# Kernel tuning notes

Hardware: AMD Instinct MI355X
Metric: run time of the kernel (lower is better)

## Reference

```python
import jax, jax.numpy as jnp
import numpy as np

THRESHOLD = 1.0
SLOPE = 25.0  # snntorch surrogate.fast_sigmoid default slope
BETA = 0.9

@jax.custom_vjp
def spike_fn(x):
    # Heaviside forward, fast-sigmoid surrogate backward: g / (slope*|x| + 1)^2
    return (x > 0).astype(x.dtype)

def _spike_fwd(x):
    return spike_fn(x), x

def _spike_bwd(x, g):
    return (g / (SLOPE * jnp.abs(x) + 1.0) ** 2,)

spike_fn.defvjp(_spike_fwd, _spike_bwd)


def setup_inputs() -> dict:
    key = jax.random.key(0)
    k_x, k_w1, k_b1, k_w2, k_b2 = jax.random.split(key, 5)
    B, T, F, H, O = 128, 256, 2500, 128, 2
    x = jax.random.normal(k_x, (B, T, F), dtype=jnp.float32)
    # PyTorch Linear init: U(-1/sqrt(fan_in), 1/sqrt(fan_in))
    s1 = 1.0 / np.sqrt(F)
    s2 = 1.0 / np.sqrt(H)
    W1 = jax.random.uniform(k_w1, (H, F), jnp.float32, -s1, s1)
    b1 = jax.random.uniform(k_b1, (H,), jnp.float32, -s1, s1)
    W2 = jax.random.uniform(k_w2, (O, H), jnp.float32, -s2, s2)
    b2 = jax.random.uniform(k_b2, (O,), jnp.float32, -s2, s2)
    return {"x": x, "W1": W1, "b1": b1, "W2": W2, "b2": b2}


def reference(x, W1, b1, W2, b2):
    # Module transposes to [time, batch, feat] when shape[0] < shape[1]
    if x.ndim == 3 and x.shape[0] < x.shape[1]:
        x = jnp.swapaxes(x, 0, 1)  # [T, B, F]
    T, B = x.shape[0], x.shape[1]
    H, O = W1.shape[0], W2.shape[0]

    def lif(mem, cur):
        # snntorch Leaky, reset_mechanism='subtract'; reset spike is detached
        rst = jax.lax.stop_gradient(spike_fn(mem - THRESHOLD))
        mem = BETA * mem + cur - rst * THRESHOLD
        spk = spike_fn(mem - THRESHOLD)
        return spk, mem

    def step(carry, xt):
        mem1, mem2 = carry
        cur1 = xt @ W1.T + b1            # [B, H]
        spk1, mem1 = lif(mem1, cur1)
        cur2 = spk1 @ W2.T + b2          # [B, O]
        spk2, mem2 = lif(mem2, cur2)
        return (mem1, mem2), (spk2, mem2)

    mem1_0 = jnp.zeros((B, H), x.dtype)
    mem2_0 = jnp.zeros((B, O), x.dtype)
    _, (spk_rec, mem_rec) = jax.lax.scan(step, (mem1_0, mem2_0), x)
    return spk_rec, mem_rec  # each [T, B, O]
```

## Files before the change

kernel.cpp:

```cpp
#include <hip/hip_runtime.h>
#include <hip/hip_bf16.h>

#define T_STEPS 256
#define B_SZ    128
#define F_SZ    2500
#define F4      625
#define NSTEP   79
#define H_SZ    128
#define O_SZ    2
#define FLAG_WINDOW 8e-5
#define CHUNK   12

typedef unsigned short U16;
typedef short  s16x8 __attribute__((ext_vector_type(8)));
typedef U16    u16x8 __attribute__((ext_vector_type(8)));
typedef float  f32x4 __attribute__((ext_vector_type(4)));

__device__ __forceinline__ U16 bf16c(float f) {
    union { __hip_bfloat16 h; U16 u; } cv;
    cv.h = __float2bfloat16(f);
    return cv.u;
}
__device__ __forceinline__ float bf2f(U16 u) { return __uint_as_float((unsigned)u << 16); }

__device__ __forceinline__ void gld16(const void* g, void* l) {
    __builtin_amdgcn_global_load_lds((const __attribute__((address_space(1))) void*)g,
                                     (__attribute__((address_space(3))) void*)l, 16, 0, 0);
}

__global__ __launch_bounds__(256) void k_split(const float* __restrict__ W1,
                                               U16* __restrict__ Wimg,
                                               int* __restrict__ nh) {
    const int bid = blockIdx.x;
    const int p = bid / NSTEP, kt = bid - p * NSTEP;
    if (bid == 0 && threadIdx.x < B_SZ) nh[threadIdx.x] = 0;
    U16* img = Wimg + ((size_t)bid << 12);
    #pragma unroll
    for (int c = 0; c < 2; ++c) {
        const int v  = c * 256 + threadIdx.x;
        const int r  = v >> 3, u = v & 7;
        const int lu = u ^ (r & 7);
        const int kb = kt * 32 + (lu & 3) * 8;
        const int h  = p * 64 + r;
        u16x8 o;
        #pragma unroll
        for (int e = 0; e < 8; ++e) {
            const int k = kb + e;
            const float w = (k < F_SZ) ? W1[(size_t)h * F_SZ + k] : 0.f;
            const U16 hi = bf16c(w);
            o[e] = (lu < 4) ? hi : bf16c(w - bf2f(hi));
        }
        *(u16x8*)(img + (size_t)v * 8) = o;
    }
}

__global__ __launch_bounds__(256, 3) void k_gemm(const float* __restrict__ x,
                                                 const U16* __restrict__ Wimg,
                                                 float* __restrict__ cur1) {
    __shared__ __align__(16) U16 Alds[2][128 * 64];
    __shared__ __align__(16) U16 Blds[2][64 * 64];

    const int g   = blockIdx.x;
    const int wg  = (g & 7) * 128 + (g >> 3);
    const int t   = wg >> 2;
    const int p   = (wg >> 1) & 1;
    const int kh  = wg & 1;
    const int kt0 = kh ? 40 : 0;
    const int nst = kh ? 39 : 40;

    const int tid = threadIdx.x;

    const int ra   = tid >> 1;
    const int kq   = (tid & 1) << 4;
    const int au0  = (tid & 1) << 1;
    const int aswz = ra & 7;
    const float* xrow = x + ((size_t)ra * T_STEPS + t) * F_SZ;

    const char* wbase = (const char*)Wimg + ((size_t)p * NSTEP << 13);

    const int lane = tid & 63, wid = tid >> 6;
    const int wm0 = (wid >> 1) << 6;
    const int wn0 = (wid & 1) << 5;
    const int lr = lane & 15, lg = lane >> 4;

    f32x4 acc[4][2];
    #pragma unroll
    for (int i = 0; i < 4; ++i)
        #pragma unroll
        for (int j = 0; j < 2; ++j) {
            acc[i][j][0] = 0.f; acc[i][j][1] = 0.f; acc[i][j][2] = 0.f; acc[i][j][3] = 0.f;
        }

    float4 xr[4];

    auto loadX = [&](int kt) {
        const int kk = kt * 32;
        #pragma unroll
        for (int c = 0; c < 4; ++c) {
            const int k = kk + kq + c * 4;
            xr[c] = (k < F_SZ) ? *(const float4*)(xrow + k) : make_float4(0.f, 0.f, 0.f, 0.f);
        }
    };
    auto loadB = [&](int kt, int bb) {
        const char* src = wbase + ((size_t)kt << 13) + (tid << 4);
        char* dst = (char*)Blds[bb] + (tid << 4);
        gld16(src, dst);
        gld16(src + 4096, dst + 4096);
    };
    auto stageA = [&](int bb) {
        U16* Ab = Alds[bb];
        #pragma unroll
        for (int pq = 0; pq < 2; ++pq) {
            const float* f0 = (const float*)&xr[pq * 2];
            const float* f1 = (const float*)&xr[pq * 2 + 1];
            u16x8 vh, vl;
            #pragma unroll
            for (int j = 0; j < 4; ++j) {
                const U16 h0v = bf16c(f0[j]);
                const U16 h1v = bf16c(f1[j]);
                vh[j]     = h0v;
                vh[4 + j] = h1v;
                vl[j]     = bf16c(f0[j] - bf2f(h0v));
                vl[4 + j] = bf16c(f1[j] - bf2f(h1v));
            }
            *(u16x8*)(Ab + ra * 64 + (((au0 + pq) ^ aswz) << 3))     = vh;
            *(u16x8*)(Ab + ra * 64 + (((au0 + pq + 4) ^ aswz) << 3)) = vl;
        }
    };

    loadB(kt0, 0);
    loadX(kt0);
    stageA(0);

    int bb = 0;
    #pragma unroll 1
    for (int s = 0; s < nst; ++s) {
        __syncthreads();
        const bool more = (s + 1 < nst);
        if (more) { loadB(kt0 + s + 1, bb ^ 1); loadX(kt0 + s + 1); }

        const U16* Ab = Alds[bb];
        const U16* Bb = Blds[bb];
        s16x8 ah[4], al[4], bh[2], bl[2];
        #pragma unroll
        for (int fi = 0; fi < 4; ++fi) {
            const int m = wm0 + fi * 16 + lr;
            const int msw = m & 7;
            ah[fi] = *(const s16x8*)(Ab + m * 64 + ((lg ^ msw) << 3));
            al[fi] = *(const s16x8*)(Ab + m * 64 + (((lg + 4) ^ msw) << 3));
        }
        #pragma unroll
        for (int fj = 0; fj < 2; ++fj) {
            const int n = wn0 + fj * 16 + lr;
            const int nsw = n & 7;
            bh[fj] = *(const s16x8*)(Bb + n * 64 + ((lg ^ nsw) << 3));
            bl[fj] = *(const s16x8*)(Bb + n * 64 + (((lg + 4) ^ nsw) << 3));
        }
        #pragma unroll
        for (int fi = 0; fi < 4; ++fi)
            #pragma unroll
            for (int fj = 0; fj < 2; ++fj) {
                acc[fi][fj] = __builtin_amdgcn_mfma_f32_16x16x32_bf16(ah[fi], bh[fj], acc[fi][fj], 0, 0, 0);
                acc[fi][fj] = __builtin_amdgcn_mfma_f32_16x16x32_bf16(ah[fi], bl[fj], acc[fi][fj], 0, 0, 0);
                acc[fi][fj] = __builtin_amdgcn_mfma_f32_16x16x32_bf16(al[fi], bh[fj], acc[fi][fj], 0, 0, 0);
                acc[fi][fj] = __builtin_amdgcn_mfma_f32_16x16x32_bf16(al[fi], bl[fj], acc[fi][fj], 0, 0, 0);
            }

        if (more) stageA(bb ^ 1);
        bb ^= 1;
    }

    float* outp = cur1 + (size_t)kh * 4194304;
    #pragma unroll
    for (int fi = 0; fi < 4; ++fi)
        #pragma unroll
        for (int fj = 0; fj < 2; ++fj) {
            const int hcol = (p << 6) + wn0 + fj * 16 + lr;
            #pragma unroll
            for (int r = 0; r < 4; ++r) {
                const int brow = wm0 + fi * 16 + lg * 4 + r;
                outp[((size_t)t * B_SZ + brow) * H_SZ + hcol] = acc[fi][fj][r];
            }
        }
}

__global__ __launch_bounds__(256) void k_lif1(float* __restrict__ cur1,
                                              const float* __restrict__ b1,
                                              unsigned long long* __restrict__ spk_bits,
                                              int* __restrict__ nh,
                                              int* __restrict__ hlist) {
    const int idx = blockIdx.x * 256 + threadIdx.x;
    const int b = idx >> 7, h = idx & 127;
    const double b1v = (double)b1[h];
    double mem = 0.0;
    bool flagged = false;
    #pragma unroll 4
    for (int t = 0; t < T_STEPS; ++t) {
        const float p0 = cur1[(size_t)t * 16384 + idx];
        const float p1 = cur1[4194304 + (size_t)t * 16384 + idx];
        const float mrg = p0 + p1;
        cur1[(size_t)t * 16384 + idx] = mrg;
        const double cur = (double)mrg + b1v;
        const double rst = (mem > 1.0) ? 1.0 : 0.0;
        mem = fma(0.9, mem, cur) - rst;
        const bool spk = (mem > 1.0);
        const unsigned long long m = __ballot(spk);
        if ((threadIdx.x & 63) == 0)
            spk_bits[((size_t)t * B_SZ + b) * 2 + ((h >> 6) & 1)] = m;
        if (!flagged && fabs(mem - 1.0) < FLAG_WINDOW) {
            flagged = true;
            int s = atomicAdd(&nh[b], 1);
            hlist[b * 128 + s] = h;
        }
    }
}

__global__ __launch_bounds__(256) void k_cur2(const unsigned long long* __restrict__ bits,
                                              const float* __restrict__ W2,
                                              const float* __restrict__ b2,
                                              double* __restrict__ cur2) {
    __shared__ float w2s[256];
    w2s[threadIdx.x] = W2[threadIdx.x];
    __syncthreads();
    const int pair = blockIdx.x * 256 + threadIdx.x;
    unsigned long long m0 = bits[(size_t)pair * 2];
    unsigned long long m1 = bits[(size_t)pair * 2 + 1];
    double v0 = (double)b2[0], v1 = (double)b2[1];
    while (m0) {
        const int i = __ffsll((long long)m0) - 1; m0 &= m0 - 1;
        v0 += (double)w2s[i]; v1 += (double)w2s[128 + i];
    }
    while (m1) {
        const int i = __ffsll((long long)m1) - 1; m1 &= m1 - 1;
        v0 += (double)w2s[64 + i]; v1 += (double)w2s[192 + i];
    }
    cur2[(size_t)pair * 2]     = v0;
    cur2[(size_t)pair * 2 + 1] = v1;
}

__global__ __launch_bounds__(256) void k_fixA(const float* __restrict__ x,
                                              const float* __restrict__ W1,
                                              const int* __restrict__ nh,
                                              const int* __restrict__ hlist,
                                              double* __restrict__ cur_fix) {
    const int b   = blockIdx.x >> 4;
    const int tch = blockIdx.x & 15;
    const int n   = nh[b];
    if (n == 0) return;

    __shared__ float w1s[CHUNK * F_SZ];
    const int tid  = threadIdx.x;
    const int wv   = tid >> 6;
    const int lane = tid & 63;

    for (int c0 = 0; c0 < n; c0 += CHUNK) {
        const int nc = (n - c0 < CHUNK) ? (n - c0) : CHUNK;
        __syncthreads();
        for (int r = 0; r < nc; ++r) {
            const int h = hlist[b * 128 + c0 + r];
            const float4* src = (const float4*)W1 + (size_t)h * F4;
            float4* dst = (float4*)(w1s + r * F_SZ);
            for (int c = tid; c < F4; c += 256) dst[c] = src[c];
        }
        __syncthreads();

        #pragma unroll 1
        for (int tt = 0; tt < 4; ++tt) {
            const int t = tch * 16 + wv * 4 + tt;
            float4 xv[10];
            const float4* xb = (const float4*)x + ((size_t)b * T_STEPS + t) * F4;
            #pragma unroll
            for (int j = 0; j < 10; ++j) {
                const int c = lane + 64 * j;
                xv[j] = (c < F4) ? xb[c] : make_float4(0.f, 0.f, 0.f, 0.f);
            }
            for (int s = 0; s < nc; ++s) {
                const float* wr = w1s + s * F_SZ;
                double p = 0.0;
                #pragma unroll
                for (int j = 0; j < 10; ++j) {
                    const int c = lane + 64 * j;
                    if (c < F4) {
                        const float4 w4 = *(const float4*)(wr + c * 4);
                        p = fma((double)xv[j].x, (double)w4.x, p);
                        p = fma((double)xv[j].y, (double)w4.y, p);
                        p = fma((double)xv[j].z, (double)w4.z, p);
                        p = fma((double)xv[j].w, (double)w4.w, p);
                    }
                }
                #pragma unroll
                for (int off = 32; off >= 1; off >>= 1) p += __shfl_down(p, off);
                if (lane == 0)
                    cur_fix[((size_t)b * 128 + c0 + s) * T_STEPS + t] = p;
            }
        }
    }
}

__global__ __launch_bounds__(128) void k_fixB(const float* __restrict__ cur1,
                                              const double* __restrict__ cur_fix,
                                              const float* __restrict__ b1,
                                              const float* __restrict__ W2,
                                              const int* __restrict__ nh,
                                              const int* __restrict__ hlist,
                                              double* __restrict__ cur2) {
    const int b = blockIdx.x;
    const int s = threadIdx.x;
    if (s >= nh[b]) return;
    const int h = hlist[b * 128 + s];
    const double b1v = (double)b1[h];
    const double w0 = (double)W2[h], w1 = (double)W2[128 + h];
    double ma = 0.0, me = 0.0;
    for (int t = 0; t < T_STEPS; ++t) {
        const double ca = (double)cur1[((size_t)t * B_SZ + b) * H_SZ + h] + b1v;
        const double ce = cur_fix[((size_t)b * 128 + s) * T_STEPS + t] + b1v;
        const double ra = (ma > 1.0) ? 1.0 : 0.0;
        const double re = (me > 1.0) ? 1.0 : 0.0;
        ma = fma(0.9, ma, ca) - ra;
        me = fma(0.9, me, ce) - re;
        const bool sa = (ma > 1.0), se = (me > 1.0);
        if (sa != se) {
            const double d = se ? 1.0 : -1.0;
            atomicAdd(&cur2[((size_t)t * B_SZ + b) * 2 + 0], d * w0);
            atomicAdd(&cur2[((size_t)t * B_SZ + b) * 2 + 1], d * w1);
        }
    }
}

__global__ __launch_bounds__(256) void k_lif2(const double* __restrict__ cur2,
                                              float* __restrict__ out) {
    const int tid = threadIdx.x;
    double mem = 0.0;
    float* spk_out = out;
    float* mem_out = out + T_STEPS * B_SZ * O_SZ;
    #pragma unroll 8
    for (int t = 0; t < T_STEPS; ++t) {
        const double cur = cur2[t * 256 + tid];
        const double rst = (mem > 1.0) ? 1.0 : 0.0;
        mem = fma(0.9, mem, cur) - rst;
        spk_out[t * 256 + tid] = (mem > 1.0) ? 1.0f : 0.0f;
        mem_out[t * 256 + tid] = (float)mem;
    }
}

extern "C" void kernel_launch(void* const* d_in, const int* in_sizes, int n_in,
                              void* d_out, int out_size, void* d_ws, size_t ws_size,
                              hipStream_t stream) {
    const float* x  = (const float*)d_in[0];
    const float* W1 = (const float*)d_in[1];
    const float* b1 = (const float*)d_in[2];
    const float* W2 = (const float*)d_in[3];
    const float* b2 = (const float*)d_in[4];
    float* out = (float*)d_out;

    char* ws = (char*)d_ws;
    float*  cur1    = (float*)ws;
    double* cur_fix = (double*)(ws + 16777216);
    U16*    Wimg    = (U16*)(ws + 50331648);
    unsigned long long* spk_bits = (unsigned long long*)(ws + 50331648);
    double* cur2    = (double*)(ws + 51625984);
    int*    nh      = (int*)(ws + 52150272);
    int*    hlist   = (int*)(ws + 52150784);

    k_split<<<158, 256, 0, stream>>>(W1, Wimg, nh);
    k_gemm<<<1024, 256, 0, stream>>>(x, Wimg, cur1);
    k_lif1<<<64, 256, 0, stream>>>(cur1, b1, spk_bits, nh, hlist);
    k_cur2<<<128, 256, 0, stream>>>(spk_bits, W2, b2, cur2);
    k_fixA<<<2048, 256, 0, stream>>>(x, W1, nh, hlist, cur_fix);
    k_fixB<<<128, 128, 0, stream>>>(cur1, cur_fix, b1, W2, nh, hlist, cur2);
    k_lif2<<<1, 256, 0, stream>>>(cur2, out);
}
```

Before: 778.9 us.

## Drop split-K, triple-buffer the GEMM pipeline and skip the lo·lo MFMA

The GEMM stops splitting K across two workgroups. Each of 512 workgroups now walks the full K range with a two-stage-ahead prefetch into triple-buffered B tiles and ping-ponged x registers. Synchronisation uses explicit waitcnt and barrier calls, and s_setprio is raised around the MFMA block. The low×low bf16 correction MFMA is removed, cutting matrix work by a quarter at a tiny precision cost, and k_lif1 no longer has to merge two partial sums. k_fixB's time loop is unrolled. Occupancy drops to 2 blocks per CU, and the manual vmcnt counting is fragile if the load count per step ever changes.

```diff
diff --git a/kernel.cpp b/kernel.cpp
--- a/kernel.cpp
+++ b/kernel.cpp
@@ -54,19 +54,16 @@
     }
 }
 
-__global__ __launch_bounds__(256, 3) void k_gemm(const float* __restrict__ x,
+__global__ __launch_bounds__(256, 2) void k_gemm(const float* __restrict__ x,
                                                  const U16* __restrict__ Wimg,
                                                  float* __restrict__ cur1) {
     __shared__ __align__(16) U16 Alds[2][128 * 64];
-    __shared__ __align__(16) U16 Blds[2][64 * 64];
-
-    const int g   = blockIdx.x;
-    const int wg  = (g & 7) * 128 + (g >> 3);
-    const int t   = wg >> 2;
-    const int p   = (wg >> 1) & 1;
-    const int kh  = wg & 1;
-    const int kt0 = kh ? 40 : 0;
-    const int nst = kh ? 39 : 40;
+    __shared__ __align__(16) U16 Blds[3][64 * 64];
+
+    const int g  = blockIdx.x;
+    const int wg = (g & 7) * 64 + (g >> 3);
+    const int t  = wg >> 1;
+    const int p  = wg & 1;
 
     const int tid = threadIdx.x;
 
@@ -91,24 +88,24 @@
             acc[i][j][0] = 0.f; acc[i][j][1] = 0.f; acc[i][j][2] = 0.f; acc[i][j][3] = 0.f;
         }
 
-    float4 xr[4];
-
-    auto loadX = [&](int kt) {
-        const int kk = kt * 32;
-        #pragma unroll
-        for (int c = 0; c < 4; ++c) {
-            const int k = kk + kq + c * 4;
-            xr[c] = (k < F_SZ) ? *(const float4*)(xrow + k) : make_float4(0.f, 0.f, 0.f, 0.f);
-        }
-    };
-    auto loadB = [&](int kt, int bb) {
+    float4 xrA[4], xrB[4];
+    const float4 f4z = make_float4(0.f, 0.f, 0.f, 0.f);
+
+    auto issueB = [&](int kt, int buf) {
         const char* src = wbase + ((size_t)kt << 13) + (tid << 4);
-        char* dst = (char*)Blds[bb] + (tid << 4);
+        char* dst = (char*)Blds[buf] + (tid << 4);
         gld16(src, dst);
         gld16(src + 4096, dst + 4096);
     };
-    auto stageA = [&](int bb) {
-        U16* Ab = Alds[bb];
+    auto issueX = [&](float4 (&xr)[4], int kt) {
+        const int kk = kt * 32 + kq;
+        xr[0] = (kk      < F_SZ) ? *(const float4*)(xrow + kk)      : f4z;
+        xr[1] = (kk + 4  < F_SZ) ? *(const float4*)(xrow + kk + 4)  : f4z;
+        xr[2] = (kk + 8  < F_SZ) ? *(const float4*)(xrow + kk + 8)  : f4z;
+        xr[3] = (kk + 12 < F_SZ) ? *(const float4*)(xrow + kk + 12) : f4z;
+    };
+    auto stageA = [&](float4 (&xr)[4], int ab) {
+        U16* Ab = Alds[ab];
         #pragma unroll
         for (int pq = 0; pq < 2; ++pq) {
             const float* f0 = (const float*)&xr[pq * 2];
@@ -128,19 +125,15 @@
         }
     };
 
-    loadB(kt0, 0);
-    loadX(kt0);
-    stageA(0);
-
-    int bb = 0;
-    #pragma unroll 1
-    for (int s = 0; s < nst; ++s) {
-        __syncthreads();
-        const bool more = (s + 1 < nst);
-        if (more) { loadB(kt0 + s + 1, bb ^ 1); loadX(kt0 + s + 1); }
-
-        const U16* Ab = Alds[bb];
-        const U16* Bb = Blds[bb];
+    int s = 0, bR = 0, bW = 2, aR = 0;
+
+    auto step = [&](float4 (&xi)[4], float4 (&xs)[4]) {
+        const int ktc = (s + 2 < NSTEP) ? s + 2 : NSTEP - 1;
+        issueB(ktc, bW);
+        issueX(xi, ktc);
+
+        const U16* Ab = Alds[aR];
+        const U16* Bb = Blds[bR];
         s16x8 ah[4], al[4], bh[2], bl[2];
         #pragma unroll
         for (int fi = 0; fi < 4; ++fi) {
@@ -156,6 +149,7 @@
             bh[fj] = *(const s16x8*)(Bb + n * 64 + ((lg ^ nsw) << 3));
             bl[fj] = *(const s16x8*)(Bb + n * 64 + (((lg + 4) ^ nsw) << 3));
         }
+        __builtin_amdgcn_s_setprio(1);
         #pragma unroll
         for (int fi = 0; fi < 4; ++fi)
             #pragma unroll
@@ -163,14 +157,35 @@
                 acc[fi][fj] = __builtin_amdgcn_mfma_f32_16x16x32_bf16(ah[fi], bh[fj], acc[fi][fj], 0, 0, 0);
                 acc[fi][fj] = __builtin_amdgcn_mfma_f32_16x16x32_bf16(ah[fi], bl[fj], acc[fi][fj], 0, 0, 0);
                 acc[fi][fj] = __builtin_amdgcn_mfma_f32_16x16x32_bf16(al[fi], bh[fj], acc[fi][fj], 0, 0, 0);
-                acc[fi][fj] = __builtin_amdgcn_mfma_f32_16x16x32_bf16(al[fi], bl[fj], acc[fi][fj], 0, 0, 0);
-            }
-
-        if (more) stageA(bb ^ 1);
-        bb ^= 1;
-    }
-
-    float* outp = cur1 + (size_t)kh * 4194304;
+            }
+        __builtin_amdgcn_s_setprio(0);
+
+        stageA(xs, aR ^ 1);
+
+        asm volatile("s_waitcnt vmcnt(6)" ::: "memory");
+        asm volatile("s_waitcnt lgkmcnt(0)" ::: "memory");
+        __builtin_amdgcn_s_barrier();
+
+        ++s;
+        bR = (bR == 2) ? 0 : bR + 1;
+        bW = (bW == 2) ? 0 : bW + 1;
+        aR ^= 1;
+    };
+
+    issueB(0, 0); issueX(xrA, 0);
+    issueB(1, 1); issueX(xrB, 1);
+    stageA(xrA, 0);
+    asm volatile("s_waitcnt vmcnt(6)" ::: "memory");
+    asm volatile("s_waitcnt lgkmcnt(0)" ::: "memory");
+    __builtin_amdgcn_s_barrier();
+
+    #pragma unroll 1
+    for (int sp = 0; sp < 39; ++sp) {
+        step(xrA, xrB);
+        step(xrB, xrA);
+    }
+    step(xrA, xrB);
+
     #pragma unroll
     for (int fi = 0; fi < 4; ++fi)
         #pragma unroll
@@ -179,12 +194,12 @@
             #pragma unroll
             for (int r = 0; r < 4; ++r) {
                 const int brow = wm0 + fi * 16 + lg * 4 + r;
-                outp[((size_t)t * B_SZ + brow) * H_SZ + hcol] = acc[fi][fj][r];
-            }
-        }
-}
-
-__global__ __launch_bounds__(256) void k_lif1(float* __restrict__ cur1,
+                cur1[((size_t)t * B_SZ + brow) * H_SZ + hcol] = acc[fi][fj][r];
+            }
+        }
+}
+
+__global__ __launch_bounds__(256) void k_lif1(const float* __restrict__ cur1,
                                               const float* __restrict__ b1,
                                               unsigned long long* __restrict__ spk_bits,
                                               int* __restrict__ nh,
@@ -196,11 +211,7 @@
     bool flagged = false;
     #pragma unroll 4
     for (int t = 0; t < T_STEPS; ++t) {
-        const float p0 = cur1[(size_t)t * 16384 + idx];
-        const float p1 = cur1[4194304 + (size_t)t * 16384 + idx];
-        const float mrg = p0 + p1;
-        cur1[(size_t)t * 16384 + idx] = mrg;
-        const double cur = (double)mrg + b1v;
+        const double cur = (double)cur1[(size_t)t * 16384 + idx] + b1v;
         const double rst = (mem > 1.0) ? 1.0 : 0.0;
         mem = fma(0.9, mem, cur) - rst;
         const bool spk = (mem > 1.0);
@@ -311,6 +322,7 @@
     const double b1v = (double)b1[h];
     const double w0 = (double)W2[h], w1 = (double)W2[128 + h];
     double ma = 0.0, me = 0.0;
+    #pragma unroll 4
     for (int t = 0; t < T_STEPS; ++t) {
         const double ca = (double)cur1[((size_t)t * B_SZ + b) * H_SZ + h] + b1v;
         const double ce = cur_fix[((size_t)b * 128 + s) * T_STEPS + t] + b1v;
@@ -363,7 +375,7 @@
     int*    hlist   = (int*)(ws + 52150784);
 
     k_split<<<158, 256, 0, stream>>>(W1, Wimg, nh);
-    k_gemm<<<1024, 256, 0, stream>>>(x, Wimg, cur1);
+    k_gemm<<<512, 256, 0, stream>>>(x, Wimg, cur1);
     k_lif1<<<64, 256, 0, stream>>>(cur1, b1, spk_bits, nh, hlist);
     k_cur2<<<128, 256, 0, stream>>>(spk_bits, W2, b2, cur2);
     k_fixA<<<2048, 256, 0, stream>>>(x, W1, nh, hlist, cur_fix);
```

Result: slower. 984.0 us (+26.3%).
